# Kernel optimization log

Measured on AMD Instinct MI355X. Metric: run time of the kernel, lower is better.

The kernel has to match this reference:

```python
import jax, jax.numpy as jnp
import numpy as np

T, N = 12, 1000          # frames, pedestrians
RNN, EMB, GS, OUT = 128, 64, 4, 5
G = GS * GS              # 16 grid cells


def lstm_cell(x, h, c, W_ih, W_hh, b_ih, b_hh):
    # PyTorch LSTMCell gate order: i, f, g, o
    gates = x @ W_ih.T + h @ W_hh.T + b_ih + b_hh
    i, f, g, o = jnp.split(gates, 4, axis=-1)
    c_new = jax.nn.sigmoid(f) * c + jax.nn.sigmoid(i) * jnp.tanh(g)
    h_new = jax.nn.sigmoid(o) * jnp.tanh(c_new)
    return h_new, c_new


def setup_inputs() -> dict:
    key = jax.random.key(0)
    ks = jax.random.split(key, 10)
    s = 0.02  # small init scale for weights
    # binary occupancy grid masks: grid[f, n, p, g] = 1 if ped p falls in cell g of ped n's neighborhood
    grids = (jax.random.uniform(ks[1], (T, N, N, G)) < 0.02).astype(jnp.float32)
    return {
        "input_data": jax.random.normal(ks[0], (T, N, 2), dtype=jnp.float32),
        "grids": grids,
        "hidden_states": jnp.zeros((N, RNN), dtype=jnp.float32),
        "cell_states": jnp.zeros((N, RNN), dtype=jnp.float32),
        "W_in": jax.random.normal(ks[2], (EMB, 2)) * s,
        "b_in": jnp.zeros((EMB,), dtype=jnp.float32),
        "W_soc": jax.random.normal(ks[3], (EMB, G * RNN)) * s,
        "b_soc": jnp.zeros((EMB,), dtype=jnp.float32),
        "W_ih": jax.random.normal(ks[4], (4 * RNN, 2 * EMB)) * s,
        "W_hh": jax.random.normal(ks[5], (4 * RNN, RNN)) * s,
        "b_ih": jnp.zeros((4 * RNN,), dtype=jnp.float32),
        "b_hh": jnp.zeros((4 * RNN,), dtype=jnp.float32),
        "W_out": jax.random.normal(ks[6], (OUT, RNN)) * s,
        "b_out": jnp.zeros((OUT,), dtype=jnp.float32),
    }


def reference(input_data, grids, hidden_states, cell_states,
              W_in, b_in, W_soc, b_soc, W_ih, W_hh, b_ih, b_hh, W_out, b_out):
    def step(carry, frame):
        h, c = carry
        x, grid = frame  # x: [N,2], grid: [N,N,G]
        # social pooling: for each node n, grid[n].T @ h  -> [G, RNN]
        social = jnp.einsum('npg,ph->ngh', grid, h).reshape(N, G * RNN)
        ie = jax.nn.relu(x @ W_in.T + b_in)           # [N, EMB]
        te = jax.nn.relu(social @ W_soc.T + b_soc)    # [N, EMB]
        emb = jnp.concatenate([ie, te], axis=-1)      # [N, 2*EMB]
        h, c = lstm_cell(emb, h, c, W_ih, W_hh, b_ih, b_hh)
        out = h @ W_out.T + b_out                     # [N, OUT]
        return (h, c), out

    (h, c), outputs = jax.lax.scan(step, (hidden_states, cell_states),
                                   (input_data, grids))
    return outputs, h, c  # outputs: [T, N, OUT]
```

## Files before the change

### kernel.cpp

```cpp
#include <hip/hip_runtime.h>
#include <hip/hip_bf16.h>


#define TT   12
#define NN   1000
#define RNNW 128
#define EMBW 64
#define GGW  16
#define OUTD 5
#define UCW  (GGW*EMBW)
#define AKW  256
#define NGATE 512
#define GROW (NN*GGW)

__device__ __forceinline__ float sigmf(float x) { return 1.f / (1.f + __expf(-x)); }

__global__ void k_init(const float* __restrict__ h0, const float* __restrict__ c0,
                       float* __restrict__ h, float* __restrict__ c) {
    int i = blockIdx.x * 256 + threadIdx.x;
    if (i < NN * RNNW) { h[i] = h0[i]; c[i] = c0[i]; }
}

__global__ __launch_bounds__(256) void k_U(const float* __restrict__ h,
                                           const float* __restrict__ Wsoc,
                                           float* __restrict__ U) {
    __shared__ float sA[32][RNNW];
    __shared__ float sB[64][RNNW + 1];
    const int tid = threadIdx.x;
    const int p0 = blockIdx.x * 32;
    const int g  = blockIdx.y;
    {
        int r = tid >> 3, c0_ = (tid & 7) * 16;
        int p = p0 + r;
        const float4 z = {0.f, 0.f, 0.f, 0.f};
        #pragma unroll
        for (int q = 0; q < 4; q++) {
            float4 v = z;
            if (p < NN) v = *(const float4*)(h + (size_t)p * RNNW + c0_ + q * 4);
            *(float4*)(&sA[r][c0_ + q * 4]) = v;
        }
    }
    {
        int e = tid >> 2, c0_ = (tid & 3) * 32;
        const float* src = Wsoc + (size_t)e * (GGW * RNNW) + g * RNNW + c0_;
        #pragma unroll
        for (int q = 0; q < 8; q++) {
            float4 v = *(const float4*)(src + q * 4);
            sB[e][c0_ + q * 4 + 0] = v.x;
            sB[e][c0_ + q * 4 + 1] = v.y;
            sB[e][c0_ + q * 4 + 2] = v.z;
            sB[e][c0_ + q * 4 + 3] = v.w;
        }
    }
    __syncthreads();
    const int tx = tid & 63, ty = tid >> 6;
    float acc[8];
    #pragma unroll
    for (int i = 0; i < 8; i++) acc[i] = 0.f;
    for (int k = 0; k < RNNW; k++) {
        float b = sB[tx][k];
        #pragma unroll
        for (int i = 0; i < 8; i++) acc[i] += sA[ty + 4 * i][k] * b;
    }
    #pragma unroll
    for (int i = 0; i < 8; i++) {
        int p = p0 + ty + 4 * i;
        if (p < NN) U[(size_t)p * UCW + g * EMBW + tx] = acc[i];
    }
}

__global__ __launch_bounds__(512) void k_pool(const unsigned int* __restrict__ grids,
                                              const float* __restrict__ x_in,
                                              const float* __restrict__ U,
                                              const float* __restrict__ h,
                                              const float* __restrict__ W_in,
                                              const float* __restrict__ b_in,
                                              const float* __restrict__ b_soc,
                                              float* __restrict__ A, int t) {
    const int n = blockIdx.x;
    const int tid = threadIdx.x;
    const int lane = tid & 63, wave = tid >> 6;
    const unsigned int* gp = grids + ((size_t)t * NN + n) * (size_t)GROW;
    float acc = 0.f;
    for (int it = 0; it < 8; ++it) {
        int base = (it * 8 + wave) * 256;
        if (base >= GROW) break;
        int f0 = base + lane * 4;
        uint4 v = {0u, 0u, 0u, 0u};
        if (f0 < GROW) v = *(const uint4*)(gp + f0);
        unsigned int va[4] = {v.x, v.y, v.z, v.w};
        #pragma unroll
        for (int sub = 0; sub < 4; ++sub) {
            unsigned long long m = __ballot(va[sub] != 0u);
            while (m) {
                int b = __builtin_ctzll(m); m &= m - 1;
                int f = base + b * 4 + sub;
                int p = f >> 4, g = f & 15;
                acc += U[(size_t)p * UCW + g * EMBW + lane];
            }
        }
    }
    __shared__ float sAcc[8][64];
    sAcc[wave][lane] = acc;
    __syncthreads();
    if (tid < 64) {
        float s = 0.f;
        #pragma unroll
        for (int w = 0; w < 8; w++) s += sAcc[w][tid];
        float te = fmaxf(s + b_soc[tid], 0.f);
        float x0 = x_in[((size_t)t * NN + n) * 2 + 0];
        float x1 = x_in[((size_t)t * NN + n) * 2 + 1];
        float ie = fmaxf(W_in[tid * 2 + 0] * x0 + W_in[tid * 2 + 1] * x1 + b_in[tid], 0.f);
        A[(size_t)n * AKW + tid] = ie;
        A[(size_t)n * AKW + EMBW + tid] = te;
    } else if (tid >= 128 && tid < 256) {
        int k = tid - 128;
        A[(size_t)n * AKW + 128 + k] = h[(size_t)n * RNNW + k];
    }
}

__global__ __launch_bounds__(256) void k_gates(const float* __restrict__ A,
                                               const float* __restrict__ W_ih,
                                               const float* __restrict__ W_hh,
                                               const float* __restrict__ b_ih,
                                               const float* __restrict__ b_hh,
                                               float* __restrict__ gates) {
    __shared__ float sA[32][128];
    __shared__ float sB[64][129];
    const int tid = threadIdx.x;
    const int n0 = blockIdx.x * 32;
    const int j0 = blockIdx.y * 64;
    const int tx = tid & 63, ty = tid >> 6;
    float acc[8];
    #pragma unroll
    for (int i = 0; i < 8; i++) acc[i] = 0.f;
    for (int kk = 0; kk < 2; ++kk) {
        __syncthreads();
        {
            int r = tid >> 3, c0_ = (tid & 7) * 16;
            int n = n0 + r;
            const float4 z = {0.f, 0.f, 0.f, 0.f};
            #pragma unroll
            for (int q = 0; q < 4; q++) {
                float4 v = z;
                if (n < NN) v = *(const float4*)(A + (size_t)n * AKW + kk * 128 + c0_ + q * 4);
                *(float4*)(&sA[r][c0_ + q * 4]) = v;
            }
        }
        {
            int e = tid >> 2, c0_ = (tid & 3) * 32;
            const float* W = kk ? W_hh : W_ih;
            const float* src = W + (size_t)(j0 + e) * 128 + c0_;
            #pragma unroll
            for (int q = 0; q < 8; q++) {
                float4 v = *(const float4*)(src + q * 4);
                sB[e][c0_ + q * 4 + 0] = v.x;
                sB[e][c0_ + q * 4 + 1] = v.y;
                sB[e][c0_ + q * 4 + 2] = v.z;
                sB[e][c0_ + q * 4 + 3] = v.w;
            }
        }
        __syncthreads();
        for (int k = 0; k < 128; k++) {
            float b = sB[tx][k];
            #pragma unroll
            for (int i = 0; i < 8; i++) acc[i] += sA[ty + 4 * i][k] * b;
        }
    }
    float bias = b_ih[j0 + tx] + b_hh[j0 + tx];
    #pragma unroll
    for (int i = 0; i < 8; i++) {
        int n = n0 + ty + 4 * i;
        if (n < NN) gates[(size_t)n * NGATE + j0 + tx] = acc[i] + bias;
    }
}

__global__ __launch_bounds__(256) void k_lstm(const float* __restrict__ gates,
                                              float* __restrict__ h, float* __restrict__ c,
                                              const float* __restrict__ W_out,
                                              const float* __restrict__ b_out,
                                              float* __restrict__ out, int t) {
    __shared__ float sh[2][128];
    int tid = threadIdx.x;
    int local = tid >> 7;
    int r = tid & 127;
    int n = blockIdx.x * 2 + local;
    float hn = 0.f;
    if (n < NN) {
        const float* gr = gates + (size_t)n * NGATE;
        float gi = gr[r], gf = gr[128 + r], gg = gr[256 + r], go = gr[384 + r];
        float cn = sigmf(gf) * c[(size_t)n * RNNW + r] + sigmf(gi) * tanhf(gg);
        hn = sigmf(go) * tanhf(cn);
        c[(size_t)n * RNNW + r] = cn;
        h[(size_t)n * RNNW + r] = hn;
    }
    sh[local][r] = hn;
    __syncthreads();
    if (n < NN && r < OUTD) {
        float s = b_out[r];
        const float* wr = W_out + r * RNNW;
        for (int k = 0; k < RNNW; k++) s += sh[local][k] * wr[k];
        out[((size_t)t * NN + n) * OUTD + r] = s;
    }
}

__global__ void k_final(const float* __restrict__ h, const float* __restrict__ c,
                        float* __restrict__ out) {
    int i = blockIdx.x * 256 + threadIdx.x;
    if (i < NN * RNNW) {
        out[TT * NN * OUTD + i] = h[i];
        out[TT * NN * OUTD + NN * RNNW + i] = c[i];
    }
}

extern "C" void kernel_launch(void* const* d_in, const int* in_sizes, int n_in,
                              void* d_out, int out_size, void* d_ws, size_t ws_size,
                              hipStream_t stream) {
    const float* x_in        = (const float*)d_in[0];
    const unsigned int* grd  = (const unsigned int*)d_in[1];
    const float* h0          = (const float*)d_in[2];
    const float* c0          = (const float*)d_in[3];
    const float* W_in        = (const float*)d_in[4];
    const float* b_in        = (const float*)d_in[5];
    const float* W_soc       = (const float*)d_in[6];
    const float* b_soc       = (const float*)d_in[7];
    const float* W_ih        = (const float*)d_in[8];
    const float* W_hh        = (const float*)d_in[9];
    const float* b_ih        = (const float*)d_in[10];
    const float* b_hh        = (const float*)d_in[11];
    const float* W_out       = (const float*)d_in[12];
    const float* b_out       = (const float*)d_in[13];
    float* out = (float*)d_out;

    float* h     = (float*)d_ws;
    float* c     = h + NN * RNNW;
    float* U     = c + NN * RNNW;
    float* A     = U + (size_t)NN * UCW;
    float* gates = A + (size_t)NN * AKW;

    hipLaunchKernelGGL(k_init, dim3(500), dim3(256), 0, stream, h0, c0, h, c);
    for (int t = 0; t < TT; ++t) {
        hipLaunchKernelGGL(k_U,     dim3(32, 16), dim3(256), 0, stream, h, W_soc, U);
        hipLaunchKernelGGL(k_pool,  dim3(NN),     dim3(512), 0, stream, grd, x_in, U, h, W_in, b_in, b_soc, A, t);
        hipLaunchKernelGGL(k_gates, dim3(32, 8),  dim3(256), 0, stream, A, W_ih, W_hh, b_ih, b_hh, gates);
        hipLaunchKernelGGL(k_lstm,  dim3(500),    dim3(256), 0, stream, gates, h, c, W_out, b_out, out, t);
    }
    hipLaunchKernelGGL(k_final, dim3(500), dim3(256), 0, stream, h, c, out);
}
```

Baseline: 734.0 us.

## Fuse all timesteps into one persistent cooperative kernel with grid syncs

Replaces the per-timestep sequence of four kernel launches with a single cooperative kernel of 250 blocks, each owning 4 pedestrians. Blocks keep h and c in shared memory and use grid.sync to order the shared U buffer between steps. The gate GEMM and LSTM update are fused per block, using transposed, pair-interleaved weights built once at kernel start. The grid-row loads in the pooling loop are software-prefetched. This removes about 50 launches and the global round-trips for A and the gates, at the cost of grid-wide barriers and lower per-block parallelism in the small GEMMs.

Result: slower. 1.832 ms (+149.5%).

```diff
diff --git a/kernel.cpp b/kernel.cpp
--- a/kernel.cpp
+++ b/kernel.cpp
@@ -1,249 +1,245 @@
 #include <hip/hip_runtime.h>
-#include <hip/hip_bf16.h>
-
-
-#define TT   12
-#define NN   1000
-#define RNNW 128
-#define EMBW 64
-#define GGW  16
-#define OUTD 5
-#define UCW  (GGW*EMBW)
-#define AKW  256
-#define NGATE 512
-#define GROW (NN*GGW)
+#include <hip/hip_cooperative_groups.h>
+
+namespace cg = cooperative_groups;
+
+
+#define TT    12
+#define NN    1000
+#define RNNW  128
+#define OUTD  5
+#define GROW  16000
+#define NB    250
+#define NTH   512
 
 __device__ __forceinline__ float sigmf(float x) { return 1.f / (1.f + __expf(-x)); }
 
-__global__ void k_init(const float* __restrict__ h0, const float* __restrict__ c0,
-                       float* __restrict__ h, float* __restrict__ c) {
-    int i = blockIdx.x * 256 + threadIdx.x;
-    if (i < NN * RNNW) { h[i] = h0[i]; c[i] = c0[i]; }
+__device__ __forceinline__ void compute_U(const float (*sH)[RNNW],
+                                          const float* __restrict__ WsT2p,
+                                          float* __restrict__ U, int n0, int tid) {
+    const int jd = tid;
+    float acc0[4] = {0.f, 0.f, 0.f, 0.f};
+    float acc1[4] = {0.f, 0.f, 0.f, 0.f};
+    for (int k = 0; k < RNNW; k += 4) {
+        float4 a[4];
+        #pragma unroll
+        for (int p = 0; p < 4; ++p) a[p] = *(const float4*)(&sH[p][k]);
+        const int r0 = (k >> 1), r1 = (k >> 1) + 1;
+        float2 w00 = *(const float2*)(WsT2p + r0 * 2048 + jd * 2);
+        float2 w01 = *(const float2*)(WsT2p + r0 * 2048 + (jd + 512) * 2);
+        float2 w10 = *(const float2*)(WsT2p + r1 * 2048 + jd * 2);
+        float2 w11 = *(const float2*)(WsT2p + r1 * 2048 + (jd + 512) * 2);
+        #pragma unroll
+        for (int p = 0; p < 4; ++p) {
+            acc0[p] += a[p].x * w00.x + a[p].y * w00.y + a[p].z * w10.x + a[p].w * w10.y;
+            acc1[p] += a[p].x * w01.x + a[p].y * w01.y + a[p].z * w11.x + a[p].w * w11.y;
+        }
+    }
+    #pragma unroll
+    for (int p = 0; p < 4; ++p) {
+        U[(size_t)(n0 + p) * 1024 + jd]       = acc0[p];
+        U[(size_t)(n0 + p) * 1024 + jd + 512] = acc1[p];
+    }
 }
 
-__global__ __launch_bounds__(256) void k_U(const float* __restrict__ h,
-                                           const float* __restrict__ Wsoc,
-                                           float* __restrict__ U) {
-    __shared__ float sA[32][RNNW];
-    __shared__ float sB[64][RNNW + 1];
-    const int tid = threadIdx.x;
-    const int p0 = blockIdx.x * 32;
-    const int g  = blockIdx.y;
+__global__ __launch_bounds__(NTH) void k_main(
+    const float* __restrict__ x_in, const unsigned int* __restrict__ grd,
+    const float* __restrict__ h0, const float* __restrict__ c0,
+    const float* __restrict__ W_in, const float* __restrict__ b_in,
+    const float* __restrict__ W_soc, const float* __restrict__ b_soc,
+    const float* __restrict__ W_ih, const float* __restrict__ W_hh,
+    const float* __restrict__ b_ih, const float* __restrict__ b_hh,
+    const float* __restrict__ W_out, const float* __restrict__ b_out,
+    float* __restrict__ U, float* __restrict__ WsT2p, float* __restrict__ WcT2p,
+    float* __restrict__ out)
+{
+    cg::grid_group grid = cg::this_grid();
+    __shared__ float sH[4][RNNW], sC[4][RNNW], sA[4][RNNW];
+    __shared__ float sG[4][512];
+    __shared__ float sAcc[8][64];
+    __shared__ float sRed[4][2][OUTD];
+
+    const int tid  = threadIdx.x;
+    const int lane = tid & 63;
+    const int b    = blockIdx.x;
+    const int n0   = b * 4;
+
+    for (int i = b * NTH + tid; i < 131072; i += NB * NTH) {
+        int e = i >> 11, gk = i & 2047, g = gk >> 7, k = gk & 127;
+        int j = g * 64 + e;
+        WsT2p[(k >> 1) * 2048 + j * 2 + (k & 1)] = W_soc[i];
+    }
+    for (int i = b * NTH + tid; i < 65536; i += NB * NTH) {
+        int j = i >> 7, k = i & 127;
+        WcT2p[(k >> 1) * 1024 + j * 2 + (k & 1)]        = W_ih[i];
+        WcT2p[((k >> 1) + 64) * 1024 + j * 2 + (k & 1)] = W_hh[i];
+    }
     {
-        int r = tid >> 3, c0_ = (tid & 7) * 16;
-        int p = p0 + r;
-        const float4 z = {0.f, 0.f, 0.f, 0.f};
-        #pragma unroll
-        for (int q = 0; q < 4; q++) {
-            float4 v = z;
-            if (p < NN) v = *(const float4*)(h + (size_t)p * RNNW + c0_ + q * 4);
-            *(float4*)(&sA[r][c0_ + q * 4]) = v;
+        int pl = tid >> 7, r = tid & 127;
+        sH[pl][r] = h0[(n0 + pl) * RNNW + r];
+        sC[pl][r] = c0[(n0 + pl) * RNNW + r];
+    }
+    __syncthreads();
+    grid.sync();
+    compute_U(sH, WsT2p, U, n0, tid);
+
+    for (int t = 0; t < TT; ++t) {
+        grid.sync();
+        {
+            const int wv = tid >> 6;
+            const int pl = wv >> 1, hf = wv & 1;
+            const unsigned int* gp = grd + (size_t)(t * NN + n0 + pl) * GROW;
+            const int fbase = hf * 8000;
+            float acc = 0.f;
+            uint4 buf[4];
+            #pragma unroll
+            for (int q = 0; q < 4; ++q) {
+                int f0 = fbase + q * 256 + lane * 4;
+                buf[q] = make_uint4(0u, 0u, 0u, 0u);
+                if (q * 256 + lane * 4 < 8000) buf[q] = *(const uint4*)(gp + f0);
+            }
+            for (int it = 0; it < 32; ++it) {
+                uint4 cur = buf[it & 3];
+                if (it + 4 < 32) {
+                    int itn = it + 4;
+                    int f0 = fbase + itn * 256 + lane * 4;
+                    uint4 nv = make_uint4(0u, 0u, 0u, 0u);
+                    if (itn * 256 + lane * 4 < 8000) nv = *(const uint4*)(gp + f0);
+                    buf[it & 3] = nv;
+                }
+                const int base = fbase + it * 256;
+                unsigned int va[4] = {cur.x, cur.y, cur.z, cur.w};
+                #pragma unroll
+                for (int sub = 0; sub < 4; ++sub) {
+                    unsigned long long m = __ballot(va[sub] != 0u);
+                    while (m) {
+                        int bb = __builtin_ctzll(m); m &= m - 1;
+                        int f = base + bb * 4 + sub;
+                        acc += U[(size_t)(f >> 4) * 1024 + (f & 15) * 64 + lane];
+                    }
+                }
+            }
+            sAcc[wv][lane] = acc;
+        }
+        __syncthreads();
+        if (tid < 256) {
+            int pl = tid >> 6, e = tid & 63;
+            float te = fmaxf(sAcc[2 * pl][e] + sAcc[2 * pl + 1][e] + b_soc[e], 0.f);
+            float x0 = x_in[(size_t)(t * NN + n0 + pl) * 2 + 0];
+            float x1 = x_in[(size_t)(t * NN + n0 + pl) * 2 + 1];
+            float ie = fmaxf(W_in[e * 2 + 0] * x0 + W_in[e * 2 + 1] * x1 + b_in[e], 0.f);
+            sA[pl][e]      = ie;
+            sA[pl][64 + e] = te;
+        }
+        __syncthreads();
+        {
+            const int jh = tid & 255, ph = tid >> 8;
+            float g00 = 0.f, g01 = 0.f, g10 = 0.f, g11 = 0.f;
+            #pragma unroll 4
+            for (int k = 0; k < 128; k += 4) {
+                float4 aA = *(const float4*)(&sA[2 * ph][k]);
+                float4 aB = *(const float4*)(&sA[2 * ph + 1][k]);
+                const int r0 = (k >> 1), r1 = (k >> 1) + 1;
+                float2 w00 = *(const float2*)(WcT2p + r0 * 1024 + jh * 2);
+                float2 w01 = *(const float2*)(WcT2p + r0 * 1024 + (jh + 256) * 2);
+                float2 w10 = *(const float2*)(WcT2p + r1 * 1024 + jh * 2);
+                float2 w11 = *(const float2*)(WcT2p + r1 * 1024 + (jh + 256) * 2);
+                g00 += aA.x * w00.x + aA.y * w00.y + aA.z * w10.x + aA.w * w10.y;
+                g01 += aA.x * w01.x + aA.y * w01.y + aA.z * w11.x + aA.w * w11.y;
+                g10 += aB.x * w00.x + aB.y * w00.y + aB.z * w10.x + aB.w * w10.y;
+                g11 += aB.x * w01.x + aB.y * w01.y + aB.z * w11.x + aB.w * w11.y;
+            }
+            #pragma unroll 4
+            for (int k = 0; k < 128; k += 4) {
+                float4 aA = *(const float4*)(&sH[2 * ph][k]);
+                float4 aB = *(const float4*)(&sH[2 * ph + 1][k]);
+                const int r0 = 64 + (k >> 1), r1 = 64 + (k >> 1) + 1;
+                float2 w00 = *(const float2*)(WcT2p + r0 * 1024 + jh * 2);
+                float2 w01 = *(const float2*)(WcT2p + r0 * 1024 + (jh + 256) * 2);
+                float2 w10 = *(const float2*)(WcT2p + r1 * 1024 + jh * 2);
+                float2 w11 = *(const float2*)(WcT2p + r1 * 1024 + (jh + 256) * 2);
+                g00 += aA.x * w00.x + aA.y * w00.y + aA.z * w10.x + aA.w * w10.y;
+                g01 += aA.x * w01.x + aA.y * w01.y + aA.z * w11.x + aA.w * w11.y;
+                g10 += aB.x * w00.x + aB.y * w00.y + aB.z * w10.x + aB.w * w10.y;
+                g11 += aB.x * w01.x + aB.y * w01.y + aB.z * w11.x + aB.w * w11.y;
+            }
+            float bias0 = b_ih[jh] + b_hh[jh];
+            float bias1 = b_ih[jh + 256] + b_hh[jh + 256];
+            sG[2 * ph][jh]           = g00 + bias0;
+            sG[2 * ph][jh + 256]     = g01 + bias1;
+            sG[2 * ph + 1][jh]       = g10 + bias0;
+            sG[2 * ph + 1][jh + 256] = g11 + bias1;
+        }
+        __syncthreads();
+        {
+            int pl = tid >> 7, r = tid & 127;
+            float gi = sG[pl][r], gf = sG[pl][128 + r];
+            float gg = sG[pl][256 + r], go = sG[pl][384 + r];
+            float cn = sigmf(gf) * sC[pl][r] + sigmf(gi) * tanhf(gg);
+            float hn = sigmf(go) * tanhf(cn);
+            sC[pl][r] = cn;
+            sH[pl][r] = hn;
+        }
+        __syncthreads();
+        {
+            int pl = tid >> 7, p128 = tid & 127, wh = (tid >> 6) & 1;
+            float v = sH[pl][p128];
+            #pragma unroll
+            for (int d = 0; d < OUTD; ++d) {
+                float pr = v * W_out[d * RNNW + p128];
+                #pragma unroll
+                for (int off = 32; off > 0; off >>= 1) pr += __shfl_down(pr, off);
+                if (lane == 0) sRed[pl][wh][d] = pr;
+            }
+        }
+        __syncthreads();
+        if (tid < 4 * OUTD) {
+            int pl = tid / OUTD, d = tid % OUTD;
+            out[((size_t)t * NN + n0 + pl) * OUTD + d] =
+                sRed[pl][0][d] + sRed[pl][1][d] + b_out[d];
+        }
+        if (t < TT - 1) {
+            __syncthreads();
+            compute_U(sH, WsT2p, U, n0, tid);
         }
     }
     {
-        int e = tid >> 2, c0_ = (tid & 3) * 32;
-        const float* src = Wsoc + (size_t)e * (GGW * RNNW) + g * RNNW + c0_;
-        #pragma unroll
-        for (int q = 0; q < 8; q++) {
-            float4 v = *(const float4*)(src + q * 4);
-            sB[e][c0_ + q * 4 + 0] = v.x;
-            sB[e][c0_ + q * 4 + 1] = v.y;
-            sB[e][c0_ + q * 4 + 2] = v.z;
-            sB[e][c0_ + q * 4 + 3] = v.w;
-        }
-    }
-    __syncthreads();
-    const int tx = tid & 63, ty = tid >> 6;
-    float acc[8];
-    #pragma unroll
-    for (int i = 0; i < 8; i++) acc[i] = 0.f;
-    for (int k = 0; k < RNNW; k++) {
-        float b = sB[tx][k];
-        #pragma unroll
-        for (int i = 0; i < 8; i++) acc[i] += sA[ty + 4 * i][k] * b;
-    }
-    #pragma unroll
-    for (int i = 0; i < 8; i++) {
-        int p = p0 + ty + 4 * i;
-        if (p < NN) U[(size_t)p * UCW + g * EMBW + tx] = acc[i];
-    }
-}
-
-__global__ __launch_bounds__(512) void k_pool(const unsigned int* __restrict__ grids,
-                                              const float* __restrict__ x_in,
-                                              const float* __restrict__ U,
-                                              const float* __restrict__ h,
-                                              const float* __restrict__ W_in,
-                                              const float* __restrict__ b_in,
-                                              const float* __restrict__ b_soc,
-                                              float* __restrict__ A, int t) {
-    const int n = blockIdx.x;
-    const int tid = threadIdx.x;
-    const int lane = tid & 63, wave = tid >> 6;
-    const unsigned int* gp = grids + ((size_t)t * NN + n) * (size_t)GROW;
-    float acc = 0.f;
-    for (int it = 0; it < 8; ++it) {
-        int base = (it * 8 + wave) * 256;
-        if (base >= GROW) break;
-        int f0 = base + lane * 4;
-        uint4 v = {0u, 0u, 0u, 0u};
-        if (f0 < GROW) v = *(const uint4*)(gp + f0);
-        unsigned int va[4] = {v.x, v.y, v.z, v.w};
-        #pragma unroll
-        for (int sub = 0; sub < 4; ++sub) {
-            unsigned long long m = __ballot(va[sub] != 0u);
-            while (m) {
-                int b = __builtin_ctzll(m); m &= m - 1;
-                int f = base + b * 4 + sub;
-                int p = f >> 4, g = f & 15;
-                acc += U[(size_t)p * UCW + g * EMBW + lane];
-            }
-        }
-    }
-    __shared__ float sAcc[8][64];
-    sAcc[wave][lane] = acc;
-    __syncthreads();
-    if (tid < 64) {
-        float s = 0.f;
-        #pragma unroll
-        for (int w = 0; w < 8; w++) s += sAcc[w][tid];
-        float te = fmaxf(s + b_soc[tid], 0.f);
-        float x0 = x_in[((size_t)t * NN + n) * 2 + 0];
-        float x1 = x_in[((size_t)t * NN + n) * 2 + 1];
-        float ie = fmaxf(W_in[tid * 2 + 0] * x0 + W_in[tid * 2 + 1] * x1 + b_in[tid], 0.f);
-        A[(size_t)n * AKW + tid] = ie;
-        A[(size_t)n * AKW + EMBW + tid] = te;
-    } else if (tid >= 128 && tid < 256) {
-        int k = tid - 128;
-        A[(size_t)n * AKW + 128 + k] = h[(size_t)n * RNNW + k];
-    }
-}
-
-__global__ __launch_bounds__(256) void k_gates(const float* __restrict__ A,
-                                               const float* __restrict__ W_ih,
-                                               const float* __restrict__ W_hh,
-                                               const float* __restrict__ b_ih,
-                                               const float* __restrict__ b_hh,
-                                               float* __restrict__ gates) {
-    __shared__ float sA[32][128];
-    __shared__ float sB[64][129];
-    const int tid = threadIdx.x;
-    const int n0 = blockIdx.x * 32;
-    const int j0 = blockIdx.y * 64;
-    const int tx = tid & 63, ty = tid >> 6;
-    float acc[8];
-    #pragma unroll
-    for (int i = 0; i < 8; i++) acc[i] = 0.f;
-    for (int kk = 0; kk < 2; ++kk) {
-        __syncthreads();
-        {
-            int r = tid >> 3, c0_ = (tid & 7) * 16;
-            int n = n0 + r;
-            const float4 z = {0.f, 0.f, 0.f, 0.f};
-            #pragma unroll
-            for (int q = 0; q < 4; q++) {
-                float4 v = z;
-                if (n < NN) v = *(const float4*)(A + (size_t)n * AKW + kk * 128 + c0_ + q * 4);
-                *(float4*)(&sA[r][c0_ + q * 4]) = v;
-            }
-        }
-        {
-            int e = tid >> 2, c0_ = (tid & 3) * 32;
-            const float* W = kk ? W_hh : W_ih;
-            const float* src = W + (size_t)(j0 + e) * 128 + c0_;
-            #pragma unroll
-            for (int q = 0; q < 8; q++) {
-                float4 v = *(const float4*)(src + q * 4);
-                sB[e][c0_ + q * 4 + 0] = v.x;
-                sB[e][c0_ + q * 4 + 1] = v.y;
-                sB[e][c0_ + q * 4 + 2] = v.z;
-                sB[e][c0_ + q * 4 + 3] = v.w;
-            }
-        }
-        __syncthreads();
-        for (int k = 0; k < 128; k++) {
-            float b = sB[tx][k];
-            #pragma unroll
-            for (int i = 0; i < 8; i++) acc[i] += sA[ty + 4 * i][k] * b;
-        }
-    }
-    float bias = b_ih[j0 + tx] + b_hh[j0 + tx];
-    #pragma unroll
-    for (int i = 0; i < 8; i++) {
-        int n = n0 + ty + 4 * i;
-        if (n < NN) gates[(size_t)n * NGATE + j0 + tx] = acc[i] + bias;
-    }
-}
-
-__global__ __launch_bounds__(256) void k_lstm(const float* __restrict__ gates,
-                                              float* __restrict__ h, float* __restrict__ c,
-                                              const float* __restrict__ W_out,
-                                              const float* __restrict__ b_out,
-                                              float* __restrict__ out, int t) {
-    __shared__ float sh[2][128];
-    int tid = threadIdx.x;
-    int local = tid >> 7;
-    int r = tid & 127;
-    int n = blockIdx.x * 2 + local;
-    float hn = 0.f;
-    if (n < NN) {
-        const float* gr = gates + (size_t)n * NGATE;
-        float gi = gr[r], gf = gr[128 + r], gg = gr[256 + r], go = gr[384 + r];
-        float cn = sigmf(gf) * c[(size_t)n * RNNW + r] + sigmf(gi) * tanhf(gg);
-        hn = sigmf(go) * tanhf(cn);
-        c[(size_t)n * RNNW + r] = cn;
-        h[(size_t)n * RNNW + r] = hn;
-    }
-    sh[local][r] = hn;
-    __syncthreads();
-    if (n < NN && r < OUTD) {
-        float s = b_out[r];
-        const float* wr = W_out + r * RNNW;
-        for (int k = 0; k < RNNW; k++) s += sh[local][k] * wr[k];
-        out[((size_t)t * NN + n) * OUTD + r] = s;
-    }
-}
-
-__global__ void k_final(const float* __restrict__ h, const float* __restrict__ c,
-                        float* __restrict__ out) {
-    int i = blockIdx.x * 256 + threadIdx.x;
-    if (i < NN * RNNW) {
-        out[TT * NN * OUTD + i] = h[i];
-        out[TT * NN * OUTD + NN * RNNW + i] = c[i];
+        int pl = tid >> 7, r = tid & 127;
+        out[(size_t)TT * NN * OUTD + (size_t)(n0 + pl) * RNNW + r] = sH[pl][r];
+        out[(size_t)TT * NN * OUTD + (size_t)NN * RNNW + (size_t)(n0 + pl) * RNNW + r] = sC[pl][r];
     }
 }
 
 extern "C" void kernel_launch(void* const* d_in, const int* in_sizes, int n_in,
                               void* d_out, int out_size, void* d_ws, size_t ws_size,
                               hipStream_t stream) {
-    const float* x_in        = (const float*)d_in[0];
-    const unsigned int* grd  = (const unsigned int*)d_in[1];
-    const float* h0          = (const float*)d_in[2];
-    const float* c0          = (const float*)d_in[3];
-    const float* W_in        = (const float*)d_in[4];
-    const float* b_in        = (const float*)d_in[5];
-    const float* W_soc       = (const float*)d_in[6];
-    const float* b_soc       = (const float*)d_in[7];
-    const float* W_ih        = (const float*)d_in[8];
-    const float* W_hh        = (const float*)d_in[9];
-    const float* b_ih        = (const float*)d_in[10];
-    const float* b_hh        = (const float*)d_in[11];
-    const float* W_out       = (const float*)d_in[12];
-    const float* b_out       = (const float*)d_in[13];
+    const float* x_in       = (const float*)d_in[0];
+    const unsigned int* grd = (const unsigned int*)d_in[1];
+    const float* h0         = (const float*)d_in[2];
+    const float* c0         = (const float*)d_in[3];
+    const float* W_in       = (const float*)d_in[4];
+    const float* b_in       = (const float*)d_in[5];
+    const float* W_soc      = (const float*)d_in[6];
+    const float* b_soc      = (const float*)d_in[7];
+    const float* W_ih       = (const float*)d_in[8];
+    const float* W_hh       = (const float*)d_in[9];
+    const float* b_ih       = (const float*)d_in[10];
+    const float* b_hh       = (const float*)d_in[11];
+    const float* W_out      = (const float*)d_in[12];
+    const float* b_out      = (const float*)d_in[13];
     float* out = (float*)d_out;
 
-    float* h     = (float*)d_ws;
-    float* c     = h + NN * RNNW;
-    float* U     = c + NN * RNNW;
-    float* A     = U + (size_t)NN * UCW;
-    float* gates = A + (size_t)NN * AKW;
-
-    hipLaunchKernelGGL(k_init, dim3(500), dim3(256), 0, stream, h0, c0, h, c);
-    for (int t = 0; t < TT; ++t) {
-        hipLaunchKernelGGL(k_U,     dim3(32, 16), dim3(256), 0, stream, h, W_soc, U);
-        hipLaunchKernelGGL(k_pool,  dim3(NN),     dim3(512), 0, stream, grd, x_in, U, h, W_in, b_in, b_soc, A, t);
-        hipLaunchKernelGGL(k_gates, dim3(32, 8),  dim3(256), 0, stream, A, W_ih, W_hh, b_ih, b_hh, gates);
-        hipLaunchKernelGGL(k_lstm,  dim3(500),    dim3(256), 0, stream, gates, h, c, W_out, b_out, out, t);
-    }
-    hipLaunchKernelGGL(k_final, dim3(500), dim3(256), 0, stream, h, c, out);
+    float* U      = (float*)d_ws;
+    float* WsT2p  = U + (size_t)NN * 1024;
+    float* WcT2p  = WsT2p + 131072;
+
+    void* args[] = {
+        (void*)&x_in, (void*)&grd, (void*)&h0, (void*)&c0,
+        (void*)&W_in, (void*)&b_in, (void*)&W_soc, (void*)&b_soc,
+        (void*)&W_ih, (void*)&W_hh, (void*)&b_ih, (void*)&b_hh,
+        (void*)&W_out, (void*)&b_out,
+        (void*)&U, (void*)&WsT2p, (void*)&WcT2p, (void*)&out
+    };
+    hipLaunchCooperativeKernel((const void*)k_main, dim3(NB), dim3(NTH),
+                               args, 0, stream);
 }
```
